# Performance work log

Hardware: AMD Instinct MI355X
Metric: run time of the kernel (lower is better)

The kernel has to match this reference:

```python
import jax, jax.numpy as jnp
import numpy as np

DIM = 512
HEADS = 8
DIM_HEAD = 64
INNER = HEADS * DIM_HEAD


def setup_inputs() -> dict:
    key = jax.random.key(0)
    k1, k2, k3, k4 = jax.random.split(key, 4)
    x = jax.random.normal(k1, (4, 8192, DIM), dtype=jnp.float32)
    # nn.Linear(dim, inner*3, bias=False): weight applied as x @ W^T; store transposed form [dim, 3*inner]
    w_qkv = jax.random.normal(k2, (DIM, 3 * INNER), dtype=jnp.float32) / np.sqrt(DIM)
    w_out = jax.random.normal(k3, (INNER, DIM), dtype=jnp.float32) / np.sqrt(INNER)
    b_out = jax.random.normal(k4, (DIM,), dtype=jnp.float32) * 0.01
    return {"x": x, "w_qkv": w_qkv, "w_out": w_out, "b_out": b_out}


def reference(x, w_qkv, w_out, b_out):
    b, n, d = x.shape
    qkv = x @ w_qkv  # [b, n, 3*inner]
    q, k, v = jnp.split(qkv, 3, axis=-1)

    def to_heads(t):
        return t.reshape(b, n, HEADS, DIM_HEAD).transpose(0, 2, 1, 3)  # [b,h,n,dh]

    q, k, v = map(to_heads, (q, k, v))
    q = jax.nn.elu(q) + 1.0
    k = jax.nn.elu(k) + 1.0
    # kv summary: [b,h,dh,dh]
    kv = jnp.einsum('bhnd,bhnm->bhdm', k, v)
    # normalizer z: [b,h,n]  (note: original does NOT apply self.scale)
    z = 1.0 / (jnp.einsum('bhnd,bhd->bhn', q, k.sum(axis=2)) + 1e-6)
    out = jnp.einsum('bhnd,bhdm->bhnm', q, kv) * z[..., None]  # [b,h,n,dh]
    out = out.transpose(0, 2, 1, 3).reshape(b, n, INNER)
    return out @ w_out + b_out
```

## Files before the change

### kernel.cpp

```cpp
#include <hip/hip_runtime.h>
#include <hip/hip_bf16.h>

#define B_SZ 4
#define SEQ 8192
#define DIM 512
#define HEADS 8
#define DH 64
#define INNER 512
#define QKV_COLS 1536
#define M_TOT (B_SZ * SEQ)
#define BHN (B_SZ * HEADS)

typedef __bf16 bf16x8 __attribute__((ext_vector_type(8)));
typedef __bf16 bf16x4 __attribute__((ext_vector_type(4)));
typedef float f32x4 __attribute__((ext_vector_type(4)));

__device__ __forceinline__ float elu1(float x) {
    return x > 0.f ? x + 1.f : __expf(x);
}

__global__ void convert_weights(const float* __restrict__ w_qkv,
                                const float* __restrict__ w_out,
                                __bf16* __restrict__ wqkv_t,
                                __bf16* __restrict__ wout_t) {
    int id = blockIdx.x * 256 + threadIdx.x;
    if (id < QKV_COLS * DIM) {
        int n = id / DIM, k = id % DIM;
        wqkv_t[id] = (__bf16)w_qkv[k * QKV_COLS + n];
    } else {
        int id2 = id - QKV_COLS * DIM;
        if (id2 < INNER * DIM) {
            int n = id2 / DIM, k = id2 % DIM;
            wout_t[id2] = (__bf16)w_out[k * DIM + n];
        }
    }
}

__launch_bounds__(256, 2)
__global__ void gemm_qkv(const float* __restrict__ x,
                         const __bf16* __restrict__ wqkv_t,
                         __bf16* __restrict__ q_ws,
                         __bf16* __restrict__ kT_ws,
                         __bf16* __restrict__ vT_ws) {
    __shared__ __attribute__((aligned(16))) __bf16 As[128][40];
    __shared__ __attribute__((aligned(16))) __bf16 Bs[128][40];
    const int tid = threadIdx.x;
    const int wid = tid >> 6;
    const int lane = tid & 63;
    const int wm = wid >> 1, wn = wid & 1;
    const int lq = lane >> 4, lr = lane & 15;
    const int m0 = blockIdx.x * 128;
    const int n0 = blockIdx.y * 128;

    f32x4 acc[4][4] = {};

    for (int kb = 0; kb < DIM; kb += 32) {
#pragma unroll
        for (int t = 0; t < 4; ++t) {
            int c = tid + t * 256;
            int row = c >> 3, kc = (c & 7) * 4;
            float4 f = *reinterpret_cast<const float4*>(
                &x[(size_t)(m0 + row) * DIM + kb + kc]);
            bf16x4 h = {(__bf16)f.x, (__bf16)f.y, (__bf16)f.z, (__bf16)f.w};
            *reinterpret_cast<bf16x4*>(&As[row][kc]) = h;
        }
#pragma unroll
        for (int t = 0; t < 2; ++t) {
            int c = tid + t * 256;
            int row = c >> 2, kc = (c & 3) * 8;
            *reinterpret_cast<bf16x8*>(&Bs[row][kc]) =
                *reinterpret_cast<const bf16x8*>(
                    &wqkv_t[(size_t)(n0 + row) * DIM + kb + kc]);
        }
        __syncthreads();
        bf16x8 af[4], bfv[4];
#pragma unroll
        for (int i = 0; i < 4; ++i)
            af[i] = *reinterpret_cast<const bf16x8*>(&As[wm * 64 + i * 16 + lr][lq * 8]);
#pragma unroll
        for (int i = 0; i < 4; ++i)
            bfv[i] = *reinterpret_cast<const bf16x8*>(&Bs[wn * 64 + i * 16 + lr][lq * 8]);
#pragma unroll
        for (int i = 0; i < 4; ++i)
#pragma unroll
            for (int j = 0; j < 4; ++j)
                acc[i][j] = __builtin_amdgcn_mfma_f32_16x16x32_bf16(
                    af[i], bfv[j], acc[i][j], 0, 0, 0);
        __syncthreads();
    }

#pragma unroll
    for (int j = 0; j < 4; ++j) {
        int col = n0 + wn * 64 + j * 16 + lr;
        int which = col / INNER;
        int within = col % INNER;
        int h = within / DH, d = within % DH;
#pragma unroll
        for (int i = 0; i < 4; ++i) {
            int row_base = m0 + wm * 64 + i * 16 + lq * 4;
            int b = row_base / SEQ;
            int seq = row_base % SEQ;
            if (which == 0) {
                size_t base = ((size_t)(b * HEADS + h) * SEQ) * DH + d;
#pragma unroll
                for (int r = 0; r < 4; ++r)
                    q_ws[base + (size_t)(seq + r) * DH] = (__bf16)elu1(acc[i][j][r]);
            } else {
                __bf16* dst = (which == 1) ? kT_ws : vT_ws;
                size_t base = ((size_t)(b * HEADS + h) * DH + d) * SEQ + seq;
                bf16x4 h4;
#pragma unroll
                for (int r = 0; r < 4; ++r) {
                    float v = acc[i][j][r];
                    h4[r] = (__bf16)((which == 1) ? elu1(v) : v);
                }
                *reinterpret_cast<bf16x4*>(&dst[base]) = h4;
            }
        }
    }
}

__launch_bounds__(256, 2)
__global__ void kv_reduce(const __bf16* __restrict__ kT,
                          const __bf16* __restrict__ vT,
                          float* __restrict__ kv_t) {
    __shared__ __attribute__((aligned(16))) __bf16 Ks[64][136];
    __shared__ __attribute__((aligned(16))) __bf16 Vs[64][136];
    const int tid = threadIdx.x;
    const int wid = tid >> 6;
    const int lane = tid & 63;
    const int lq = lane >> 4, lr = lane & 15;
    const int bh = blockIdx.y;
    const int n0 = blockIdx.x * 512;
    const size_t base = (size_t)bh * DH * SEQ;
    f32x4 acc[4] = {};

    for (int ch = 0; ch < 4; ++ch) {
        int nc = n0 + ch * 128;
#pragma unroll
        for (int t = 0; t < 4; ++t) {
            int c = tid + t * 256;
            int row = c >> 4, kc = (c & 15) * 8;
            *reinterpret_cast<bf16x8*>(&Ks[row][kc]) =
                *reinterpret_cast<const bf16x8*>(&kT[base + (size_t)row * SEQ + nc + kc]);
            *reinterpret_cast<bf16x8*>(&Vs[row][kc]) =
                *reinterpret_cast<const bf16x8*>(&vT[base + (size_t)row * SEQ + nc + kc]);
        }
        __syncthreads();
#pragma unroll
        for (int ks = 0; ks < 4; ++ks) {
            bf16x8 a = *reinterpret_cast<const bf16x8*>(&Ks[wid * 16 + lr][ks * 32 + lq * 8]);
#pragma unroll
            for (int j = 0; j < 4; ++j) {
                bf16x8 b = *reinterpret_cast<const bf16x8*>(&Vs[j * 16 + lr][ks * 32 + lq * 8]);
                acc[j] = __builtin_amdgcn_mfma_f32_16x16x32_bf16(a, b, acc[j], 0, 0, 0);
            }
        }
        __syncthreads();
    }
    float* dst = kv_t + (size_t)bh * DH * DH;
#pragma unroll
    for (int j = 0; j < 4; ++j) {
        int m = j * 16 + lr;
#pragma unroll
        for (int r = 0; r < 4; ++r) {
            int d = wid * 16 + lq * 4 + r;
            atomicAdd(&dst[m * DH + d], acc[j][r]);
        }
    }
}

__global__ void ksum_kernel(const __bf16* __restrict__ kT, float* __restrict__ ksum) {
    const int wid = threadIdx.x >> 6, lane = threadIdx.x & 63;
    const int row = blockIdx.x * 4 + wid;
    const __bf16* src = kT + (size_t)row * SEQ;
    float s = 0.f;
    for (int i = 0; i < 16; ++i) {
        bf16x8 v = *reinterpret_cast<const bf16x8*>(&src[(i * 64 + lane) * 8]);
#pragma unroll
        for (int j = 0; j < 8; ++j) s += (float)v[j];
    }
#pragma unroll
    for (int off = 32; off > 0; off >>= 1) s += __shfl_down(s, off, 64);
    if (lane == 0) ksum[row] = s;
}

__launch_bounds__(256, 2)
__global__ void attn_kernel(const __bf16* __restrict__ q_ws,
                            const float* __restrict__ kv_t,
                            const float* __restrict__ ksum,
                            __bf16* __restrict__ attn) {
    __shared__ __attribute__((aligned(16))) __bf16 Qs[128][72];
    __shared__ __attribute__((aligned(16))) __bf16 KVs[64][72];
    __shared__ float zs[128];
    __shared__ float ks_s[64];
    const int tid = threadIdx.x;
    const int wid = tid >> 6, lane = tid & 63;
    const int lq = lane >> 4, lr = lane & 15;
    const int bh = blockIdx.y;
    const int b = bh >> 3, h = bh & 7;
    const int n0 = blockIdx.x * 128;
    const size_t qbase = ((size_t)bh * SEQ + n0) * DH;

#pragma unroll
    for (int t = 0; t < 4; ++t) {
        int c = tid + t * 256;
        int row = c >> 3, kc = (c & 7) * 8;
        *reinterpret_cast<bf16x8*>(&Qs[row][kc]) =
            *reinterpret_cast<const bf16x8*>(&q_ws[qbase + (size_t)row * DH + kc]);
    }
    const float* kvsrc = kv_t + (size_t)bh * DH * DH;
#pragma unroll
    for (int t = 0; t < 4; ++t) {
        int c = tid + t * 256;
        int m = c >> 4, dc = (c & 15) * 4;
        float4 f = *reinterpret_cast<const float4*>(&kvsrc[m * DH + dc]);
        bf16x4 h4 = {(__bf16)f.x, (__bf16)f.y, (__bf16)f.z, (__bf16)f.w};
        *reinterpret_cast<bf16x4*>(&KVs[m][dc]) = h4;
    }
    if (tid < 64) ks_s[tid] = ksum[bh * DH + tid];
    __syncthreads();
    {
        int row = tid >> 1, part = tid & 1;
        float s = 0.f;
#pragma unroll
        for (int j = 0; j < 32; ++j)
            s += (float)Qs[row][part * 32 + j] * ks_s[part * 32 + j];
        s += __shfl_xor(s, 1, 64);
        if (part == 0) zs[row] = 1.f / (s + 1e-6f);
    }
    __syncthreads();

    f32x4 acc[2][4] = {};
#pragma unroll
    for (int ks = 0; ks < 2; ++ks) {
        bf16x8 a0 = *reinterpret_cast<const bf16x8*>(&Qs[wid * 32 + lr][ks * 32 + lq * 8]);
        bf16x8 a1 = *reinterpret_cast<const bf16x8*>(&Qs[wid * 32 + 16 + lr][ks * 32 + lq * 8]);
#pragma unroll
        for (int j = 0; j < 4; ++j) {
            bf16x8 bfr = *reinterpret_cast<const bf16x8*>(&KVs[j * 16 + lr][ks * 32 + lq * 8]);
            acc[0][j] = __builtin_amdgcn_mfma_f32_16x16x32_bf16(a0, bfr, acc[0][j], 0, 0, 0);
            acc[1][j] = __builtin_amdgcn_mfma_f32_16x16x32_bf16(a1, bfr, acc[1][j], 0, 0, 0);
        }
    }
#pragma unroll
    for (int mt = 0; mt < 2; ++mt)
#pragma unroll
        for (int j = 0; j < 4; ++j) {
            int m = j * 16 + lr;
#pragma unroll
            for (int r = 0; r < 4; ++r) {
                int row = wid * 32 + mt * 16 + lq * 4 + r;
                float v = acc[mt][j][r] * zs[row];
                attn[((size_t)(b * SEQ + n0 + row)) * INNER + h * DH + m] = (__bf16)v;
            }
        }
}

__launch_bounds__(256, 2)
__global__ void gemm_out(const __bf16* __restrict__ attn,
                         const __bf16* __restrict__ wout_t,
                         const float* __restrict__ b_out,
                         float* __restrict__ out) {
    __shared__ __attribute__((aligned(16))) __bf16 As[128][40];
    __shared__ __attribute__((aligned(16))) __bf16 Bs[128][40];
    const int tid = threadIdx.x;
    const int wid = tid >> 6;
    const int lane = tid & 63;
    const int wm = wid >> 1, wn = wid & 1;
    const int lq = lane >> 4, lr = lane & 15;
    const int m0 = blockIdx.x * 128;
    const int n0 = blockIdx.y * 128;

    f32x4 acc[4][4] = {};

    for (int kb = 0; kb < INNER; kb += 32) {
#pragma unroll
        for (int t = 0; t < 2; ++t) {
            int c = tid + t * 256;
            int row = c >> 2, kc = (c & 3) * 8;
            *reinterpret_cast<bf16x8*>(&As[row][kc]) =
                *reinterpret_cast<const bf16x8*>(
                    &attn[(size_t)(m0 + row) * INNER + kb + kc]);
        }
#pragma unroll
        for (int t = 0; t < 2; ++t) {
            int c = tid + t * 256;
            int row = c >> 2, kc = (c & 3) * 8;
            *reinterpret_cast<bf16x8*>(&Bs[row][kc]) =
                *reinterpret_cast<const bf16x8*>(
                    &wout_t[(size_t)(n0 + row) * INNER + kb + kc]);
        }
        __syncthreads();
        bf16x8 af[4], bfv[4];
#pragma unroll
        for (int i = 0; i < 4; ++i)
            af[i] = *reinterpret_cast<const bf16x8*>(&As[wm * 64 + i * 16 + lr][lq * 8]);
#pragma unroll
        for (int i = 0; i < 4; ++i)
            bfv[i] = *reinterpret_cast<const bf16x8*>(&Bs[wn * 64 + i * 16 + lr][lq * 8]);
#pragma unroll
        for (int i = 0; i < 4; ++i)
#pragma unroll
            for (int j = 0; j < 4; ++j)
                acc[i][j] = __builtin_amdgcn_mfma_f32_16x16x32_bf16(
                    af[i], bfv[j], acc[i][j], 0, 0, 0);
        __syncthreads();
    }

#pragma unroll
    for (int j = 0; j < 4; ++j) {
        int col = n0 + wn * 64 + j * 16 + lr;
        float bias = b_out[col];
#pragma unroll
        for (int i = 0; i < 4; ++i) {
            int row = m0 + wm * 64 + i * 16 + lq * 4;
#pragma unroll
            for (int r = 0; r < 4; ++r)
                out[(size_t)(row + r) * DIM + col] = acc[i][j][r] + bias;
        }
    }
}

extern "C" void kernel_launch(void* const* d_in, const int* in_sizes, int n_in,
                              void* d_out, int out_size, void* d_ws, size_t ws_size,
                              hipStream_t stream) {
    (void)in_sizes; (void)n_in; (void)out_size; (void)ws_size;
    const float* x     = (const float*)d_in[0];
    const float* w_qkv = (const float*)d_in[1];
    const float* w_out = (const float*)d_in[2];
    const float* b_out = (const float*)d_in[3];
    float* out = (float*)d_out;

    char* ws = (char*)d_ws;
    size_t off = 0;
    auto alloc = [&](size_t bytes) {
        char* p = ws + off;
        off += (bytes + 255) & ~(size_t)255;
        return p;
    };
    __bf16* q_ws   = (__bf16*)alloc((size_t)BHN * SEQ * DH * 2);
    __bf16* kT_ws  = (__bf16*)alloc((size_t)BHN * SEQ * DH * 2);
    __bf16* vT_ws  = (__bf16*)alloc((size_t)BHN * SEQ * DH * 2);
    __bf16* attn   = (__bf16*)alloc((size_t)M_TOT * INNER * 2);
    float*  kv_t   = (float*)alloc((size_t)BHN * DH * DH * 4 + (size_t)BHN * DH * 4);
    float*  ksum   = kv_t + (size_t)BHN * DH * DH;
    __bf16* wqkv_t = (__bf16*)alloc((size_t)QKV_COLS * DIM * 2);
    __bf16* wout_t = (__bf16*)alloc((size_t)INNER * DIM * 2);

    hipMemsetAsync(kv_t, 0, (size_t)BHN * DH * DH * 4 + (size_t)BHN * DH * 4, stream);
    convert_weights<<<dim3((QKV_COLS * DIM + INNER * DIM) / 256), 256, 0, stream>>>(
        w_qkv, w_out, wqkv_t, wout_t);
    gemm_qkv<<<dim3(M_TOT / 128, QKV_COLS / 128), 256, 0, stream>>>(
        x, wqkv_t, q_ws, kT_ws, vT_ws);
    kv_reduce<<<dim3(16, BHN), 256, 0, stream>>>(kT_ws, vT_ws, kv_t);
    ksum_kernel<<<dim3(BHN * DH / 4), 256, 0, stream>>>(kT_ws, ksum);
    attn_kernel<<<dim3(SEQ / 128, BHN), 256, 0, stream>>>(q_ws, kv_t, ksum, attn);
    gemm_out<<<dim3(M_TOT / 128, DIM / 128), 256, 0, stream>>>(attn, wout_t, b_out, out);
}
```

Baseline: 296.4 us.

## Pre-convert x to bf16, use direct global-to-LDS loads, and stage epilogue through LDS

x is converted to bf16 once in a separate kernel, so the QKV GEMM no longer reads fp32 x and converts it 12 times (once per N tile). Both GEMMs now load tiles straight into LDS with global_load_lds (16B per lane) and use K=64 per iteration. The QKV epilogue stages the tile through LDS and transposes it, so q/kT/vT are written with 16-byte coalesced stores instead of scattered 2- or 8-byte stores. The LDS tiles are unpadded, which may cause bank conflicts on the MFMA fragment reads, and the attn buffer now reuses the xb workspace.

```diff
diff --git a/kernel.cpp b/kernel.cpp
--- a/kernel.cpp
+++ b/kernel.cpp
@@ -17,6 +17,19 @@
 
 __device__ __forceinline__ float elu1(float x) {
     return x > 0.f ? x + 1.f : __expf(x);
+}
+
+__device__ __forceinline__ void gl_lds16(const void* g, void* l) {
+    __builtin_amdgcn_global_load_lds(
+        (const __attribute__((address_space(1))) unsigned int*)g,
+        (__attribute__((address_space(3))) unsigned int*)l, 16, 0, 0);
+}
+
+__global__ void convert_x(const float* __restrict__ x, __bf16* __restrict__ xb) {
+    int id = blockIdx.x * 256 + threadIdx.x;
+    float4 f = reinterpret_cast<const float4*>(x)[id];
+    bf16x4 h = {(__bf16)f.x, (__bf16)f.y, (__bf16)f.z, (__bf16)f.w};
+    reinterpret_cast<bf16x4*>(xb)[id] = h;
 }
 
 __global__ void convert_weights(const float* __restrict__ w_qkv,
@@ -36,14 +49,18 @@
     }
 }
 
+#define TSTR 136
 __launch_bounds__(256, 2)
-__global__ void gemm_qkv(const float* __restrict__ x,
+__global__ void gemm_qkv(const __bf16* __restrict__ xb,
                          const __bf16* __restrict__ wqkv_t,
                          __bf16* __restrict__ q_ws,
                          __bf16* __restrict__ kT_ws,
                          __bf16* __restrict__ vT_ws) {
-    __shared__ __attribute__((aligned(16))) __bf16 As[128][40];
-    __shared__ __attribute__((aligned(16))) __bf16 Bs[128][40];
+    __shared__ __attribute__((aligned(16))) char smem[128 * TSTR * 2];
+    __bf16* As = (__bf16*)smem;
+    __bf16* Bs = (__bf16*)(smem + 16384);
+    __bf16* T  = (__bf16*)smem;
+
     const int tid = threadIdx.x;
     const int wid = tid >> 6;
     const int lane = tid & 63;
@@ -51,71 +68,94 @@
     const int lq = lane >> 4, lr = lane & 15;
     const int m0 = blockIdx.x * 128;
     const int n0 = blockIdx.y * 128;
+    const int lrow = lane >> 3;
+    const int lcol = (lane & 7) * 8;
 
     f32x4 acc[4][4] = {};
 
-    for (int kb = 0; kb < DIM; kb += 32) {
+    for (int kb = 0; kb < DIM; kb += 64) {
 #pragma unroll
         for (int t = 0; t < 4; ++t) {
-            int c = tid + t * 256;
-            int row = c >> 3, kc = (c & 7) * 4;
-            float4 f = *reinterpret_cast<const float4*>(
-                &x[(size_t)(m0 + row) * DIM + kb + kc]);
-            bf16x4 h = {(__bf16)f.x, (__bf16)f.y, (__bf16)f.z, (__bf16)f.w};
-            *reinterpret_cast<bf16x4*>(&As[row][kc]) = h;
-        }
-#pragma unroll
-        for (int t = 0; t < 2; ++t) {
-            int c = tid + t * 256;
-            int row = c >> 2, kc = (c & 3) * 8;
-            *reinterpret_cast<bf16x8*>(&Bs[row][kc]) =
-                *reinterpret_cast<const bf16x8*>(
-                    &wqkv_t[(size_t)(n0 + row) * DIM + kb + kc]);
-        }
-        __syncthreads();
-        bf16x8 af[4], bfv[4];
+            int qi = wid * 4 + t;
+            int row = qi * 8 + lrow;
+            gl_lds16(&xb[(size_t)(m0 + row) * DIM + kb + lcol], &As[qi * 512]);
+            gl_lds16(&wqkv_t[(size_t)(n0 + row) * DIM + kb + lcol], &Bs[qi * 512]);
+        }
+        __syncthreads();
+#pragma unroll
+        for (int ks = 0; ks < 2; ++ks) {
+            bf16x8 af[4], bfv[4];
+#pragma unroll
+            for (int i = 0; i < 4; ++i)
+                af[i] = *reinterpret_cast<const bf16x8*>(
+                    &As[(wm * 64 + i * 16 + lr) * 64 + ks * 32 + lq * 8]);
+#pragma unroll
+            for (int j = 0; j < 4; ++j)
+                bfv[j] = *reinterpret_cast<const bf16x8*>(
+                    &Bs[(wn * 64 + j * 16 + lr) * 64 + ks * 32 + lq * 8]);
+#pragma unroll
+            for (int i = 0; i < 4; ++i)
+#pragma unroll
+                for (int j = 0; j < 4; ++j)
+                    acc[i][j] = __builtin_amdgcn_mfma_f32_16x16x32_bf16(
+                        af[i], bfv[j], acc[i][j], 0, 0, 0);
+        }
+        __syncthreads();
+    }
+
+    const int which = n0 / INNER;
+    const int n0w = n0 % INNER;
+    const int b = m0 / SEQ;
+    const int nbase = m0 % SEQ;
+
+    if (which == 0) {
 #pragma unroll
         for (int i = 0; i < 4; ++i)
-            af[i] = *reinterpret_cast<const bf16x8*>(&As[wm * 64 + i * 16 + lr][lq * 8]);
+#pragma unroll
+            for (int j = 0; j < 4; ++j) {
+                int col = wn * 64 + j * 16 + lr;
+#pragma unroll
+                for (int r = 0; r < 4; ++r)
+                    T[(wm * 64 + i * 16 + lq * 4 + r) * TSTR + col] =
+                        (__bf16)elu1(acc[i][j][r]);
+            }
+        __syncthreads();
+#pragma unroll
+        for (int it = 0; it < 8; ++it) {
+            int c = tid + it * 256;
+            int row = c >> 4, dc = (c & 15) * 8;
+            bf16x8 v = *reinterpret_cast<const bf16x8*>(&T[row * TSTR + dc]);
+            int col = n0w + dc;
+            int h = col >> 6, d = col & 63;
+            *reinterpret_cast<bf16x8*>(
+                &q_ws[(((size_t)(b * HEADS + h)) * SEQ + nbase + row) * DH + d]) = v;
+        }
+    } else {
+        __bf16* dst = (which == 1) ? kT_ws : vT_ws;
 #pragma unroll
         for (int i = 0; i < 4; ++i)
-            bfv[i] = *reinterpret_cast<const bf16x8*>(&Bs[wn * 64 + i * 16 + lr][lq * 8]);
-#pragma unroll
-        for (int i = 0; i < 4; ++i)
-#pragma unroll
-            for (int j = 0; j < 4; ++j)
-                acc[i][j] = __builtin_amdgcn_mfma_f32_16x16x32_bf16(
-                    af[i], bfv[j], acc[i][j], 0, 0, 0);
-        __syncthreads();
-    }
-
-#pragma unroll
-    for (int j = 0; j < 4; ++j) {
-        int col = n0 + wn * 64 + j * 16 + lr;
-        int which = col / INNER;
-        int within = col % INNER;
-        int h = within / DH, d = within % DH;
-#pragma unroll
-        for (int i = 0; i < 4; ++i) {
-            int row_base = m0 + wm * 64 + i * 16 + lq * 4;
-            int b = row_base / SEQ;
-            int seq = row_base % SEQ;
-            if (which == 0) {
-                size_t base = ((size_t)(b * HEADS + h) * SEQ) * DH + d;
-#pragma unroll
-                for (int r = 0; r < 4; ++r)
-                    q_ws[base + (size_t)(seq + r) * DH] = (__bf16)elu1(acc[i][j][r]);
-            } else {
-                __bf16* dst = (which == 1) ? kT_ws : vT_ws;
-                size_t base = ((size_t)(b * HEADS + h) * DH + d) * SEQ + seq;
+#pragma unroll
+            for (int j = 0; j < 4; ++j) {
+                int col = wn * 64 + j * 16 + lr;
+                int rowb = wm * 64 + i * 16 + lq * 4;
                 bf16x4 h4;
 #pragma unroll
                 for (int r = 0; r < 4; ++r) {
                     float v = acc[i][j][r];
                     h4[r] = (__bf16)((which == 1) ? elu1(v) : v);
                 }
-                *reinterpret_cast<bf16x4*>(&dst[base]) = h4;
+                *reinterpret_cast<bf16x4*>(&T[col * TSTR + rowb]) = h4;
             }
+        __syncthreads();
+#pragma unroll
+        for (int it = 0; it < 8; ++it) {
+            int c = tid + it * 256;
+            int colIdx = c >> 4, rc = (c & 15) * 8;
+            bf16x8 v = *reinterpret_cast<const bf16x8*>(&T[colIdx * TSTR + rc]);
+            int gcol = n0w + colIdx;
+            int h = gcol >> 6, d = gcol & 63;
+            *reinterpret_cast<bf16x8*>(
+                &dst[(((size_t)(b * HEADS + h)) * DH + d) * SEQ + nbase + rc]) = v;
         }
     }
 }
@@ -262,8 +302,10 @@
                          const __bf16* __restrict__ wout_t,
                          const float* __restrict__ b_out,
                          float* __restrict__ out) {
-    __shared__ __attribute__((aligned(16))) __bf16 As[128][40];
-    __shared__ __attribute__((aligned(16))) __bf16 Bs[128][40];
+    __shared__ __attribute__((aligned(16))) char smem[32768];
+    __bf16* As = (__bf16*)smem;
+    __bf16* Bs = (__bf16*)(smem + 16384);
+
     const int tid = threadIdx.x;
     const int wid = tid >> 6;
     const int lane = tid & 63;
@@ -271,40 +313,38 @@
     const int lq = lane >> 4, lr = lane & 15;
     const int m0 = blockIdx.x * 128;
     const int n0 = blockIdx.y * 128;
+    const int lrow = lane >> 3;
+    const int lcol = (lane & 7) * 8;
 
     f32x4 acc[4][4] = {};
 
-    for (int kb = 0; kb < INNER; kb += 32) {
-#pragma unroll
-        for (int t = 0; t < 2; ++t) {
-            int c = tid + t * 256;
-            int row = c >> 2, kc = (c & 3) * 8;
-            *reinterpret_cast<bf16x8*>(&As[row][kc]) =
-                *reinterpret_cast<const bf16x8*>(
-                    &attn[(size_t)(m0 + row) * INNER + kb + kc]);
-        }
-#pragma unroll
-        for (int t = 0; t < 2; ++t) {
-            int c = tid + t * 256;
-            int row = c >> 2, kc = (c & 3) * 8;
-            *reinterpret_cast<bf16x8*>(&Bs[row][kc]) =
-                *reinterpret_cast<const bf16x8*>(
-                    &wout_t[(size_t)(n0 + row) * INNER + kb + kc]);
-        }
-        __syncthreads();
-        bf16x8 af[4], bfv[4];
-#pragma unroll
-        for (int i = 0; i < 4; ++i)
-            af[i] = *reinterpret_cast<const bf16x8*>(&As[wm * 64 + i * 16 + lr][lq * 8]);
-#pragma unroll
-        for (int i = 0; i < 4; ++i)
-            bfv[i] = *reinterpret_cast<const bf16x8*>(&Bs[wn * 64 + i * 16 + lr][lq * 8]);
-#pragma unroll
-        for (int i = 0; i < 4; ++i)
+    for (int kb = 0; kb < INNER; kb += 64) {
+#pragma unroll
+        for (int t = 0; t < 4; ++t) {
+            int qi = wid * 4 + t;
+            int row = qi * 8 + lrow;
+            gl_lds16(&attn[(size_t)(m0 + row) * INNER + kb + lcol], &As[qi * 512]);
+            gl_lds16(&wout_t[(size_t)(n0 + row) * INNER + kb + lcol], &Bs[qi * 512]);
+        }
+        __syncthreads();
+#pragma unroll
+        for (int ks = 0; ks < 2; ++ks) {
+            bf16x8 af[4], bfv[4];
+#pragma unroll
+            for (int i = 0; i < 4; ++i)
+                af[i] = *reinterpret_cast<const bf16x8*>(
+                    &As[(wm * 64 + i * 16 + lr) * 64 + ks * 32 + lq * 8]);
 #pragma unroll
             for (int j = 0; j < 4; ++j)
-                acc[i][j] = __builtin_amdgcn_mfma_f32_16x16x32_bf16(
-                    af[i], bfv[j], acc[i][j], 0, 0, 0);
+                bfv[j] = *reinterpret_cast<const bf16x8*>(
+                    &Bs[(wn * 64 + j * 16 + lr) * 64 + ks * 32 + lq * 8]);
+#pragma unroll
+            for (int i = 0; i < 4; ++i)
+#pragma unroll
+                for (int j = 0; j < 4; ++j)
+                    acc[i][j] = __builtin_amdgcn_mfma_f32_16x16x32_bf16(
+                        af[i], bfv[j], acc[i][j], 0, 0, 0);
+        }
         __syncthreads();
     }
 
@@ -339,20 +379,22 @@
         off += (bytes + 255) & ~(size_t)255;
         return p;
     };
+    __bf16* xb     = (__bf16*)alloc((size_t)M_TOT * DIM * 2);
+    __bf16* attn   = xb;
     __bf16* q_ws   = (__bf16*)alloc((size_t)BHN * SEQ * DH * 2);
     __bf16* kT_ws  = (__bf16*)alloc((size_t)BHN * SEQ * DH * 2);
     __bf16* vT_ws  = (__bf16*)alloc((size_t)BHN * SEQ * DH * 2);
-    __bf16* attn   = (__bf16*)alloc((size_t)M_TOT * INNER * 2);
     float*  kv_t   = (float*)alloc((size_t)BHN * DH * DH * 4 + (size_t)BHN * DH * 4);
     float*  ksum   = kv_t + (size_t)BHN * DH * DH;
     __bf16* wqkv_t = (__bf16*)alloc((size_t)QKV_COLS * DIM * 2);
     __bf16* wout_t = (__bf16*)alloc((size_t)INNER * DIM * 2);
 
     hipMemsetAsync(kv_t, 0, (size_t)BHN * DH * DH * 4 + (size_t)BHN * DH * 4, stream);
+    convert_x<<<dim3(M_TOT * DIM / 4 / 256), 256, 0, stream>>>(x, xb);
     convert_weights<<<dim3((QKV_COLS * DIM + INNER * DIM) / 256), 256, 0, stream>>>(
         w_qkv, w_out, wqkv_t, wout_t);
     gemm_qkv<<<dim3(M_TOT / 128, QKV_COLS / 128), 256, 0, stream>>>(
-        x, wqkv_t, q_ws, kT_ws, vT_ws);
+        xb, wqkv_t, q_ws, kT_ws, vT_ws);
     kv_reduce<<<dim3(16, BHN), 256, 0, stream>>>(kT_ws, vT_ws, kv_t);
     ksum_kernel<<<dim3(BHN * DH / 4), 256, 0, stream>>>(kT_ws, ksum);
     attn_kernel<<<dim3(SEQ / 128, BHN), 256, 0, stream>>>(q_ws, kv_t, ksum, attn);
```

New measurement: 302.7 us. +2.1%, slower.
